# Kernel tuning notes

Hardware: AMD Instinct MI355X
Metric: run time of the kernel (lower is better)

The kernel has to match this reference:

```python
import jax, jax.numpy as jnp
import numpy as np

D_MODEL = 1024
N_HEADS = 16
HEAD_DIM = D_MODEL // N_HEADS


def setup_inputs() -> dict:
    key = jax.random.key(0)
    k0, k1, k2, k3, k4, k5 = jax.random.split(key, 6)
    s = 1.0 / np.sqrt(D_MODEL)
    return {
        "q": jax.random.normal(k0, (2, 2048, D_MODEL), dtype=jnp.float32),
        "Wq": jax.random.normal(k1, (D_MODEL, D_MODEL), dtype=jnp.float32) * s,
        "Wk": jax.random.normal(k2, (D_MODEL, D_MODEL), dtype=jnp.float32) * s,
        "Wv": jax.random.normal(k3, (D_MODEL, D_MODEL), dtype=jnp.float32) * s,
        "Wo": jax.random.normal(k4, (D_MODEL, D_MODEL), dtype=jnp.float32) * s,
        "bo": jax.random.normal(k5, (D_MODEL,), dtype=jnp.float32) * 0.01,
    }


def _split_heads(x):
    b, s, _ = x.shape
    return x.reshape(b, s, N_HEADS, HEAD_DIM).transpose(0, 2, 1, 3)  # [b,h,s,d]


def reference(q, Wq, Wk, Wv, Wo, bo):
    # self-attention: k = v = q
    qh = _split_heads(q @ Wq)  # [b,h,s,d]
    kh = _split_heads(q @ Wk)
    vh = _split_heads(q @ Wv)
    scale = 1.0 / np.sqrt(HEAD_DIM).astype(np.float32)
    scores = jnp.einsum("bhqd,bhkd->bhqk", qh, kh) * scale
    attn = jax.nn.softmax(scores, axis=-1)
    ctx = jnp.einsum("bhqk,bhkd->bhqd", attn, vh)
    b, h, s, d = ctx.shape
    ctx = ctx.transpose(0, 2, 1, 3).reshape(b, s, h * d)
    return ctx @ Wo + bo
```

## Files before the change

### kernel.cpp

```cpp
#include <hip/hip_runtime.h>
#include <cstdint>

typedef unsigned short u16;
typedef __bf16 bf16x8 __attribute__((ext_vector_type(8)));
typedef __bf16 bf16x2 __attribute__((ext_vector_type(2)));
typedef float floatx4 __attribute__((ext_vector_type(4)));
typedef unsigned short u16x4 __attribute__((ext_vector_type(4)));
typedef unsigned short u16x8 __attribute__((ext_vector_type(8)));

#define MFMA16(a, b, c) __builtin_amdgcn_mfma_f32_16x16x32_bf16((a), (b), (c), 0, 0, 0)
#define QSCALE_LOG2E 0.18033688011112042f


typedef __attribute__((address_space(3))) void as3_void;
typedef __attribute__((address_space(1))) void as1_void;

static __device__ __forceinline__ void async_load16(const void* g, void* l) {
  __builtin_amdgcn_global_load_lds((as1_void*)(uintptr_t)g, (as3_void*)(uintptr_t)l,
                                   16, 0, 0);
}

static __device__ __forceinline__ u16 f2bf(float f) {
  union { float f; unsigned int u; } v; v.f = f;
  unsigned int u = v.u;
  u += 0x7fffu + ((u >> 16) & 1u);
  return (u16)(u >> 16);
}

static __device__ __forceinline__ u16x4 pack_bf4(float a, float b, float c, float d) {
#if __has_builtin(__builtin_amdgcn_cvt_pk_bf16_f32)
  union { u16x4 v4; bf16x2 v2[2]; } u;
  u.v2[0] = __builtin_amdgcn_cvt_pk_bf16_f32(a, b);
  u.v2[1] = __builtin_amdgcn_cvt_pk_bf16_f32(c, d);
  return u.v4;
#else
  u16x4 r; r[0] = f2bf(a); r[1] = f2bf(b); r[2] = f2bf(c); r[3] = f2bf(d);
  return r;
#endif
}

static __device__ __forceinline__ float fast_exp2(float x) {
#if __has_builtin(__builtin_amdgcn_exp2f)
  return __builtin_amdgcn_exp2f(x);
#else
  return exp2f(x);
#endif
}


__global__ __launch_bounds__(256) void prep_kernel(
    const float* __restrict__ w0, const float* __restrict__ w1,
    const float* __restrict__ w2, const float* __restrict__ w3,
    u16* __restrict__ wout,
    const float* __restrict__ xin, u16* __restrict__ xout) {
  if (blockIdx.z == 4) {
    int blk = blockIdx.y * 16 + blockIdx.x;
    size_t base = (size_t)blk * 16384 + (size_t)threadIdx.x * 8;
#pragma unroll
    for (int r = 0; r < 8; r++) {
      size_t i = base + (size_t)r * 2048;
      float4 a = *(const float4*)(xin + i);
      float4 b = *(const float4*)(xin + i + 4);
      u16x8 o;
      o[0] = f2bf(a.x); o[1] = f2bf(a.y); o[2] = f2bf(a.z); o[3] = f2bf(a.w);
      o[4] = f2bf(b.x); o[5] = f2bf(b.y); o[6] = f2bf(b.z); o[7] = f2bf(b.w);
      *(u16x8*)(xout + i) = o;
    }
    return;
  }
  __shared__ u16 t[64][65];
  const float* in = (blockIdx.z == 0) ? w0 : (blockIdx.z == 1) ? w1
                    : (blockIdx.z == 2) ? w2 : w3;
  u16* oz = wout + (size_t)blockIdx.z * (1024 * 1024);
  const int tid = threadIdx.x;
  const int x = tid & 63, y0 = tid >> 6;
  const int bx = blockIdx.x * 64, by = blockIdx.y * 64;
#pragma unroll
  for (int p = 0; p < 16; p++) {
    int y = y0 + p * 4;
    t[y][x] = f2bf(in[(size_t)(by + y) * 1024 + bx + x]);
  }
  __syncthreads();
#pragma unroll
  for (int p = 0; p < 16; p++) {
    int r = y0 + p * 4;
    oz[(size_t)(bx + r) * 1024 + by + x] = t[x][r];
  }
}


__global__ __launch_bounds__(256, 3) void gemm_qkv_kernel(
    const u16* __restrict__ A, const u16* __restrict__ BT,
    u16* __restrict__ out, u16* __restrict__ outVT) {
  __shared__ u16 As[128 * 32];
  __shared__ u16 Bs[128 * 32];
  __shared__ u16 tb[64 * 136];
  const int tid = threadIdx.x;
  const int w = tid >> 6, lane = tid & 63;
  const int bm = blockIdx.y * 128, bn = blockIdx.x * 128;
  const int z = blockIdx.z;
  const int K = 1024, N = 1024;
  const u16* Bz = BT + (size_t)z * N * K;

  const int c0 = w * 2, c1 = c0 + 1;
  const int mA0 = c0 * 16 + (lane >> 2), mA1 = c1 * 16 + (lane >> 2);
  const int kg0 = (lane & 3) ^ ((mA0 >> 1) & 3);
  const int kg1 = (lane & 3) ^ ((mA1 >> 1) & 3);
  const u16* agp0 = A + (size_t)(bm + mA0) * K + kg0 * 8;
  const u16* agp1 = A + (size_t)(bm + mA1) * K + kg1 * 8;
  const u16* bgp0 = Bz + (size_t)(bn + mA0) * K + kg0 * 8;
  const u16* bgp1 = Bz + (size_t)(bn + mA1) * K + kg1 * 8;
  u16* ald0 = As + c0 * 512; u16* ald1 = As + c1 * 512;
  u16* bld0 = Bs + c0 * 512; u16* bld1 = Bs + c1 * 512;

  const int wm = (w >> 1) * 64, wn = (w & 1) * 64;
  floatx4 acc[4][4] = {};

  int a_off[4], b_off[4];
#pragma unroll
  for (int i = 0; i < 4; i++) {
    int m = wm + i * 16 + (lane & 15);
    a_off[i] = m * 32 + (((lane >> 4) ^ ((m >> 1) & 3)) * 8);
    int n = wn + i * 16 + (lane & 15);
    b_off[i] = n * 32 + (((lane >> 4) ^ ((n >> 1) & 3)) * 8);
  }

  for (int k0 = 0; k0 < K; k0 += 32) {
    __syncthreads();
    async_load16(agp0 + k0, ald0);
    async_load16(agp1 + k0, ald1);
    async_load16(bgp0 + k0, bld0);
    async_load16(bgp1 + k0, bld1);
    __syncthreads();
    bf16x8 af[4], bf[4];
#pragma unroll
    for (int i = 0; i < 4; i++) af[i] = *(const bf16x8*)(As + a_off[i]);
#pragma unroll
    for (int j = 0; j < 4; j++) bf[j] = *(const bf16x8*)(Bs + b_off[j]);
#pragma unroll
    for (int i = 0; i < 4; i++)
#pragma unroll
      for (int j = 0; j < 4; j++)
        acc[i][j] = MFMA16(af[i], bf[j], acc[i][j]);
  }

  const int roff = (lane >> 4) * 4;
  const int coff = lane & 15;
  if (z == 2) {
    const int b = bm >> 11, s0 = bm & 2047;
#pragma unroll
    for (int half = 0; half < 2; half++) {
      __syncthreads();
      if ((w & 1) == half) {
#pragma unroll
        for (int i = 0; i < 4; i++) {
          int s_local = wm + i * 16 + roff;
#pragma unroll
          for (int j = 0; j < 4; j++) {
            int c_local = j * 16 + coff;
            u16x4 pk = pack_bf4(acc[i][j][0], acc[i][j][1],
                                acc[i][j][2], acc[i][j][3]);
            *(u16x4*)(tb + c_local * 136 + s_local) = pk;
          }
        }
      }
      __syncthreads();
#pragma unroll
      for (int p = 0; p < 4; p++) {
        int c_local = (tid >> 4) & 15;
        int row = p * 16 + c_local;
        int so = tid & 15;
        int cg = bn + half * 64 + row;
        int h = cg >> 6, d = cg & 63;
        u16x8 vv = *(const u16x8*)(tb + row * 136 + so * 8);
        *(u16x8*)(outVT + ((size_t)(b * 16 + h) * 64 + d) * 2048 + s0 + so * 8) = vv;
      }
    }
  } else {
    const float sc = (z == 0) ? QSCALE_LOG2E : 1.0f;
    u16* outz = out + (size_t)z * 4096 * 1024;
#pragma unroll
    for (int i = 0; i < 4; i++) {
      int r0 = bm + wm + i * 16 + roff;
#pragma unroll
      for (int j = 0; j < 4; j++) {
        int c = bn + wn + j * 16 + coff;
#pragma unroll
        for (int r = 0; r < 4; r++)
          outz[(size_t)(r0 + r) * N + c] = f2bf(acc[i][j][r] * sc);
      }
    }
  }
}


__global__ __launch_bounds__(256, 2) void gemm_o_kernel(
    const u16* __restrict__ A, const u16* __restrict__ BT,
    const float* __restrict__ bias, float* __restrict__ out) {
  __shared__ u16 As[128 * 32];
  __shared__ u16 Bs[64 * 32];
  const int tid = threadIdx.x;
  const int w = tid >> 6, lane = tid & 63;
  const int bm = blockIdx.y * 128, bn = blockIdx.x * 64;
  const int K = 1024, N = 1024;

  const u16* gp[3]; u16* ld[3];
#pragma unroll
  for (int i = 0; i < 3; i++) {
    int c = w * 3 + i;
    if (c < 8) {
      int m = c * 16 + (lane >> 2);
      int kg = (lane & 3) ^ ((m >> 1) & 3);
      gp[i] = A + (size_t)(bm + m) * K + kg * 8;
      ld[i] = As + c * 512;
    } else {
      int cb = c - 8;
      int n = cb * 16 + (lane >> 2);
      int kg = (lane & 3) ^ ((n >> 1) & 3);
      gp[i] = BT + (size_t)(bn + n) * K + kg * 8;
      ld[i] = Bs + cb * 512;
    }
  }

  const int wm = (w >> 1) * 64, wn = (w & 1) * 32;
  floatx4 acc[4][2] = {};

  int a_off[4], b_off[2];
#pragma unroll
  for (int i = 0; i < 4; i++) {
    int m = wm + i * 16 + (lane & 15);
    a_off[i] = m * 32 + (((lane >> 4) ^ ((m >> 1) & 3)) * 8);
  }
#pragma unroll
  for (int j = 0; j < 2; j++) {
    int n = wn + j * 16 + (lane & 15);
    b_off[j] = n * 32 + (((lane >> 4) ^ ((n >> 1) & 3)) * 8);
  }

  for (int k0 = 0; k0 < K; k0 += 32) {
    __syncthreads();
    async_load16(gp[0] + k0, ld[0]);
    async_load16(gp[1] + k0, ld[1]);
    async_load16(gp[2] + k0, ld[2]);
    __syncthreads();
    bf16x8 af[4], bf[2];
#pragma unroll
    for (int i = 0; i < 4; i++) af[i] = *(const bf16x8*)(As + a_off[i]);
#pragma unroll
    for (int j = 0; j < 2; j++) bf[j] = *(const bf16x8*)(Bs + b_off[j]);
#pragma unroll
    for (int i = 0; i < 4; i++)
#pragma unroll
      for (int j = 0; j < 2; j++)
        acc[i][j] = MFMA16(af[i], bf[j], acc[i][j]);
  }

  const int roff = (lane >> 4) * 4;
  const int coff = lane & 15;
#pragma unroll
  for (int i = 0; i < 4; i++) {
    int r0 = bm + wm + i * 16 + roff;
#pragma unroll
    for (int j = 0; j < 2; j++) {
      int c = bn + wn + j * 16 + coff;
      float bv = bias[c];
#pragma unroll
      for (int r = 0; r < 4; r++)
        out[(size_t)(r0 + r) * N + c] = acc[i][j][r] + bv;
    }
  }
}


__global__ __launch_bounds__(256, 3) void attn_kernel(
    const u16* __restrict__ Q, const u16* __restrict__ Kx,
    const u16* __restrict__ VT, u16* __restrict__ ctx) {
  __shared__ u16 Ks[128 * 64];
  __shared__ u16 Vs[64 * 128];
  __shared__ u16 Ps[4][32 * 72];
  const int tid = threadIdx.x;
  const int w = tid >> 6, lane = tid & 63;
  const int bid = blockIdx.x;
  const int bh = (bid >> 7) * 8 + (bid & 7);
  const int q0 = ((bid >> 3) & 15) * 128;
  const int b = bh >> 4, h = bh & 15;
  const u16* Qh = Q + (size_t)b * 2048 * 1024 + h * 64;
  const u16* Kh = Kx + (size_t)b * 2048 * 1024 + h * 64;
  const u16* Vh = VT + (size_t)bh * 64 * 2048;

  const int qbase = q0 + w * 32;
  bf16x8 qf[2][2];
#pragma unroll
  for (int qt = 0; qt < 2; qt++)
#pragma unroll
    for (int ks = 0; ks < 2; ks++)
      qf[qt][ks] = *(const bf16x8*)(Qh + (size_t)(qbase + qt * 16 + (lane & 15)) * 1024 +
                                    ks * 32 + (lane >> 4) * 8);

  bf16x8 onesf;
#pragma unroll
  for (int i = 0; i < 8; i++) onesf[i] = (__bf16)1.0f;
  const floatx4 zero4 = {};

  const u16* kgp[4]; const u16* vgp[4];
  u16* kld[4]; u16* vld[4];
#pragma unroll
  for (int i = 0; i < 4; i++) {
    int c = w * 4 + i;
    int sl = c * 8 + (lane >> 3);
    int dg = (lane & 7) ^ (lane >> 3);
    kgp[i] = Kh + (size_t)sl * 1024 + dg * 8;
    kld[i] = Ks + c * 512;
    int dl = c * 4 + (lane >> 4);
    int sg = (lane & 15) ^ (dl & 15);
    vgp[i] = Vh + (size_t)dl * 2048 + sg * 8;
    vld[i] = Vs + c * 512;
  }

  const int slot_k0 = (lane >> 4) ^ (lane & 7);
  const int slot_k1 = (4 + (lane >> 4)) ^ (lane & 7);
  const u16* kf0_base = Ks + (lane & 15) * 64 + slot_k0 * 8;
  const u16* kf1_base = Ks + (lane & 15) * 64 + slot_k1 * 8;

  floatx4 o[2][4] = {};
  floatx4 lacc[2] = {};
  u16* Pw = Ps[w];
  const int qrow0 = (lane & 15) * 72;
  const int qrow1 = (16 + (lane & 15)) * 72;
  const int quad = lane >> 4;

  for (int t = 0; t < 16; t++) {
    const int k0 = t * 128;
    __syncthreads();
#pragma unroll
    for (int i = 0; i < 4; i++) {
      async_load16(kgp[i] + (size_t)k0 * 1024, kld[i]);
      async_load16(vgp[i] + k0, vld[i]);
    }
    __syncthreads();

#pragma unroll
    for (int hh = 0; hh < 2; hh++) {
      floatx4 st0[4], st1[4];
#pragma unroll
      for (int si4 = 0; si4 < 4; si4++) {
        int si = hh * 4 + si4;
        bf16x8 kf0 = *(const bf16x8*)(kf0_base + si * 1024);
        bf16x8 kf1 = *(const bf16x8*)(kf1_base + si * 1024);
        st0[si4] = MFMA16(kf1, qf[0][1], MFMA16(kf0, qf[0][0], zero4));
        st1[si4] = MFMA16(kf1, qf[1][1], MFMA16(kf0, qf[1][0], zero4));
      }
#pragma unroll
      for (int si4 = 0; si4 < 4; si4++) {
        u16x4 pk0 = pack_bf4(fast_exp2(st0[si4][0]), fast_exp2(st0[si4][1]),
                             fast_exp2(st0[si4][2]), fast_exp2(st0[si4][3]));
        u16x4 pk1 = pack_bf4(fast_exp2(st1[si4][0]), fast_exp2(st1[si4][1]),
                             fast_exp2(st1[si4][2]), fast_exp2(st1[si4][3]));
        *(u16x4*)(Pw + qrow0 + si4 * 16 + quad * 4) = pk0;
        *(u16x4*)(Pw + qrow1 + si4 * 16 + quad * 4) = pk1;
      }
#pragma unroll
      for (int ksl = 0; ksl < 2; ksl++) {
        int kb = hh * 2 + ksl;
        bf16x8 vf[4];
#pragma unroll
        for (int jt = 0; jt < 4; jt++) {
          int d = jt * 16 + (lane & 15);
          int slot = (kb * 4 + quad) ^ (d & 15);
          vf[jt] = *(const bf16x8*)(Vs + d * 128 + slot * 8);
        }
#pragma unroll
        for (int qt = 0; qt < 2; qt++) {
          bf16x8 pf = *(const bf16x8*)(Pw + (qt * 16 + (lane & 15)) * 72 +
                                       ksl * 32 + quad * 8);
#pragma unroll
          for (int jt = 0; jt < 4; jt++)
            o[qt][jt] = MFMA16(pf, vf[jt], o[qt][jt]);
          lacc[qt] = MFMA16(pf, onesf, lacc[qt]);
        }
      }
    }
  }

#pragma unroll
  for (int qt = 0; qt < 2; qt++)
#pragma unroll
    for (int r = 0; r < 4; r++) {
      float inv = 1.0f / lacc[qt][r];
      int s = qbase + qt * 16 + quad * 4 + r;
#pragma unroll
      for (int j = 0; j < 4; j++) {
        int c = h * 64 + j * 16 + (lane & 15);
        ctx[(size_t)(b * 2048 + s) * 1024 + c] = f2bf(o[qt][j][r] * inv);
      }
    }
}


extern "C" void kernel_launch(void* const* d_in, const int* in_sizes, int n_in,
                              void* d_out, int out_size, void* d_ws, size_t ws_size,
                              hipStream_t stream) {
  (void)in_sizes; (void)n_in; (void)out_size; (void)ws_size;
  const float* x  = (const float*)d_in[0];
  const float* Wq = (const float*)d_in[1];
  const float* Wk = (const float*)d_in[2];
  const float* Wv = (const float*)d_in[3];
  const float* Wo = (const float*)d_in[4];
  const float* bo = (const float*)d_in[5];
  u16* ws = (u16*)d_ws;
  const size_t MM = 1024 * 1024;
  u16* WT  = ws;
  u16* WoT = ws + 3 * MM;
  u16* Xb  = ws + 4 * MM;
  u16* QKV = ws + 8 * MM;
  u16* VTp = ws + 20 * MM;
  u16* CTX = ws + 24 * MM;

  dim3 blk(256);
  prep_kernel<<<dim3(16, 16, 5), blk, 0, stream>>>(Wq, Wk, Wv, Wo, WT, x, Xb);
  gemm_qkv_kernel<<<dim3(8, 32, 3), blk, 0, stream>>>(Xb, WT, QKV, VTp);
  attn_kernel<<<dim3(512, 1, 1), blk, 0, stream>>>(QKV, QKV + 4 * MM, VTp, CTX);
  gemm_o_kernel<<<dim3(16, 32, 1), blk, 0, stream>>>(CTX, WoT, bo, (float*)d_out);
}
```

Measured before the change: 186.4 us.

## Prefetch next K/V tile into registers while computing current tile

Replaces the synchronous global-to-LDS async loads at the top of each iteration with register prefetching. The next tile's K and V are loaded into registers before compute and written to LDS after it, so global memory latency can overlap with the MFMA work. The extra live registers lead to lowering the launch bounds occupancy hint from 3 to 2 blocks per CU. Fewer resident waves reduces latency hiding from other blocks.

```diff
diff --git a/kernel.cpp b/kernel.cpp
--- a/kernel.cpp
+++ b/kernel.cpp
@@ -272,7 +272,7 @@
 }
 
 
-__global__ __launch_bounds__(256, 3) void attn_kernel(
+__global__ __launch_bounds__(256, 2) void attn_kernel(
     const u16* __restrict__ Q, const u16* __restrict__ Kx,
     const u16* __restrict__ VT, u16* __restrict__ ctx) {
   __shared__ u16 Ks[128 * 64];
@@ -310,11 +310,11 @@
     int sl = c * 8 + (lane >> 3);
     int dg = (lane & 7) ^ (lane >> 3);
     kgp[i] = Kh + (size_t)sl * 1024 + dg * 8;
-    kld[i] = Ks + c * 512;
+    kld[i] = Ks + c * 512 + lane * 8;
     int dl = c * 4 + (lane >> 4);
     int sg = (lane & 15) ^ (dl & 15);
     vgp[i] = Vh + (size_t)dl * 2048 + sg * 8;
-    vld[i] = Vs + c * 512;
+    vld[i] = Vs + c * 512 + lane * 8;
   }
 
   const int slot_k0 = (lane >> 4) ^ (lane & 7);
@@ -329,15 +329,28 @@
   const int qrow1 = (16 + (lane & 15)) * 72;
   const int quad = lane >> 4;
 
+  u16x8 kreg[4], vreg[4];
+#pragma unroll
+  for (int i = 0; i < 4; i++) {
+    kreg[i] = *(const u16x8*)(kgp[i]);
+    vreg[i] = *(const u16x8*)(vgp[i]);
+  }
+#pragma unroll
+  for (int i = 0; i < 4; i++) {
+    *(u16x8*)(kld[i]) = kreg[i];
+    *(u16x8*)(vld[i]) = vreg[i];
+  }
+  __syncthreads();
+
   for (int t = 0; t < 16; t++) {
-    const int k0 = t * 128;
-    __syncthreads();
-#pragma unroll
-    for (int i = 0; i < 4; i++) {
-      async_load16(kgp[i] + (size_t)k0 * 1024, kld[i]);
-      async_load16(vgp[i] + k0, vld[i]);
-    }
-    __syncthreads();
+    if (t < 15) {
+      const size_t k1 = (size_t)(t + 1) * 128;
+#pragma unroll
+      for (int i = 0; i < 4; i++) {
+        kreg[i] = *(const u16x8*)(kgp[i] + k1 * 1024);
+        vreg[i] = *(const u16x8*)(vgp[i] + k1);
+      }
+    }
 
 #pragma unroll
     for (int hh = 0; hh < 2; hh++) {
@@ -379,6 +392,16 @@
           lacc[qt] = MFMA16(pf, onesf, lacc[qt]);
         }
       }
+    }
+
+    if (t < 15) {
+      __syncthreads();
+#pragma unroll
+      for (int i = 0; i < 4; i++) {
+        *(u16x8*)(kld[i]) = kreg[i];
+        *(u16x8*)(vld[i]) = vreg[i];
+      }
+      __syncthreads();
     }
   }
 
```

Result: no change. 187.2 us (+0.4%).

## Split attention work across warps by query and key halves with LDS reduction

Applied to the files above, without the earlier changes.

Each warp now handles 64 query rows against half of the 128-key tile, instead of 32 query rows against the full tile. Partial O and row-sum accumulators from the two key-half warps are combined through LDS at the end. The point is to raise reuse of each K/V fragment read from LDS across more query tiles, cutting LDS reads per MFMA. In exchange register pressure roughly doubles (occupancy hint drops from 3 to 2 blocks), and the epilogue gains an extra LDS reduction and barrier.

```diff
diff --git a/kernel.cpp b/kernel.cpp
--- a/kernel.cpp
+++ b/kernel.cpp
@@ -272,14 +272,16 @@
 }
 
 
-__global__ __launch_bounds__(256, 3) void attn_kernel(
+__global__ __launch_bounds__(256, 2) void attn_kernel(
     const u16* __restrict__ Q, const u16* __restrict__ Kx,
     const u16* __restrict__ VT, u16* __restrict__ ctx) {
-  __shared__ u16 Ks[128 * 64];
-  __shared__ u16 Vs[64 * 128];
-  __shared__ u16 Ps[4][32 * 72];
+  __shared__ __align__(16) u16 lds[8192 + 8192 + 4 * 64 * 68];
+  u16* Ks = lds;
+  u16* Vs = lds + 8192;
+  u16* Ps = lds + 16384;
   const int tid = threadIdx.x;
   const int w = tid >> 6, lane = tid & 63;
+  const int qh = w >> 1, sh = w & 1;
   const int bid = blockIdx.x;
   const int bh = (bid >> 7) * 8 + (bid & 7);
   const int q0 = ((bid >> 3) & 15) * 128;
@@ -287,15 +289,16 @@
   const u16* Qh = Q + (size_t)b * 2048 * 1024 + h * 64;
   const u16* Kh = Kx + (size_t)b * 2048 * 1024 + h * 64;
   const u16* Vh = VT + (size_t)bh * 64 * 2048;
-
-  const int qbase = q0 + w * 32;
-  bf16x8 qf[2][2];
-#pragma unroll
-  for (int qt = 0; qt < 2; qt++)
+  const int quad = lane >> 4;
+
+  const int qbase = q0 + qh * 64;
+  bf16x8 qf[4][2];
+#pragma unroll
+  for (int qt = 0; qt < 4; qt++)
 #pragma unroll
     for (int ks = 0; ks < 2; ks++)
       qf[qt][ks] = *(const bf16x8*)(Qh + (size_t)(qbase + qt * 16 + (lane & 15)) * 1024 +
-                                    ks * 32 + (lane >> 4) * 8);
+                                    ks * 32 + quad * 8);
 
   bf16x8 onesf;
 #pragma unroll
@@ -311,89 +314,111 @@
     int dg = (lane & 7) ^ (lane >> 3);
     kgp[i] = Kh + (size_t)sl * 1024 + dg * 8;
     kld[i] = Ks + c * 512;
-    int dl = c * 4 + (lane >> 4);
+    int dl = c * 4 + quad;
     int sg = (lane & 15) ^ (dl & 15);
     vgp[i] = Vh + (size_t)dl * 2048 + sg * 8;
     vld[i] = Vs + c * 512;
   }
 
-  const int slot_k0 = (lane >> 4) ^ (lane & 7);
-  const int slot_k1 = (4 + (lane >> 4)) ^ (lane & 7);
-  const u16* kf0_base = Ks + (lane & 15) * 64 + slot_k0 * 8;
-  const u16* kf1_base = Ks + (lane & 15) * 64 + slot_k1 * 8;
-
-  floatx4 o[2][4] = {};
-  floatx4 lacc[2] = {};
-  u16* Pw = Ps[w];
-  const int qrow0 = (lane & 15) * 72;
-  const int qrow1 = (16 + (lane & 15)) * 72;
-  const int quad = lane >> 4;
+  const int slot_k0 = quad ^ (lane & 7);
+  const int slot_k1 = (4 + quad) ^ (lane & 7);
+  const u16* kf0_base = Ks + sh * 4096 + (lane & 15) * 64 + slot_k0 * 8;
+  const u16* kf1_base = Ks + sh * 4096 + (lane & 15) * 64 + slot_k1 * 8;
+
+  floatx4 o[4][4] = {};
+  floatx4 lacc[4] = {};
+  u16* Pw = Ps + w * (64 * 68);
+  int qrow[4];
+#pragma unroll
+  for (int qt = 0; qt < 4; qt++) qrow[qt] = (qt * 16 + (lane & 15)) * 68;
 
   for (int t = 0; t < 16; t++) {
-    const int k0 = t * 128;
+    const size_t k0 = (size_t)t * 128;
     __syncthreads();
 #pragma unroll
     for (int i = 0; i < 4; i++) {
-      async_load16(kgp[i] + (size_t)k0 * 1024, kld[i]);
+      async_load16(kgp[i] + k0 * 1024, kld[i]);
       async_load16(vgp[i] + k0, vld[i]);
     }
     __syncthreads();
 
-#pragma unroll
-    for (int hh = 0; hh < 2; hh++) {
-      floatx4 st0[4], st1[4];
-#pragma unroll
-      for (int si4 = 0; si4 < 4; si4++) {
-        int si = hh * 4 + si4;
-        bf16x8 kf0 = *(const bf16x8*)(kf0_base + si * 1024);
-        bf16x8 kf1 = *(const bf16x8*)(kf1_base + si * 1024);
-        st0[si4] = MFMA16(kf1, qf[0][1], MFMA16(kf0, qf[0][0], zero4));
-        st1[si4] = MFMA16(kf1, qf[1][1], MFMA16(kf0, qf[1][0], zero4));
-      }
-#pragma unroll
-      for (int si4 = 0; si4 < 4; si4++) {
-        u16x4 pk0 = pack_bf4(fast_exp2(st0[si4][0]), fast_exp2(st0[si4][1]),
-                             fast_exp2(st0[si4][2]), fast_exp2(st0[si4][3]));
-        u16x4 pk1 = pack_bf4(fast_exp2(st1[si4][0]), fast_exp2(st1[si4][1]),
-                             fast_exp2(st1[si4][2]), fast_exp2(st1[si4][3]));
-        *(u16x4*)(Pw + qrow0 + si4 * 16 + quad * 4) = pk0;
-        *(u16x4*)(Pw + qrow1 + si4 * 16 + quad * 4) = pk1;
-      }
-#pragma unroll
-      for (int ksl = 0; ksl < 2; ksl++) {
-        int kb = hh * 2 + ksl;
-        bf16x8 vf[4];
-#pragma unroll
-        for (int jt = 0; jt < 4; jt++) {
-          int d = jt * 16 + (lane & 15);
-          int slot = (kb * 4 + quad) ^ (d & 15);
-          vf[jt] = *(const bf16x8*)(Vs + d * 128 + slot * 8);
+    floatx4 st[4][4];
+#pragma unroll
+    for (int si = 0; si < 4; si++) {
+      bf16x8 kf0 = *(const bf16x8*)(kf0_base + si * 1024);
+      bf16x8 kf1 = *(const bf16x8*)(kf1_base + si * 1024);
+#pragma unroll
+      for (int qt = 0; qt < 4; qt++)
+        st[si][qt] = MFMA16(kf1, qf[qt][1], MFMA16(kf0, qf[qt][0], zero4));
+    }
+#pragma unroll
+    for (int si = 0; si < 4; si++)
+#pragma unroll
+      for (int qt = 0; qt < 4; qt++) {
+        u16x4 pk = pack_bf4(fast_exp2(st[si][qt][0]), fast_exp2(st[si][qt][1]),
+                            fast_exp2(st[si][qt][2]), fast_exp2(st[si][qt][3]));
+        *(u16x4*)(Pw + qrow[qt] + si * 16 + quad * 4) = pk;
+      }
+
+#pragma unroll
+    for (int ksl = 0; ksl < 2; ksl++) {
+      int kb = sh * 2 + ksl;
+      bf16x8 vf[4];
+#pragma unroll
+      for (int jt = 0; jt < 4; jt++) {
+        int d = jt * 16 + (lane & 15);
+        int slot = (kb * 4 + quad) ^ (d & 15);
+        vf[jt] = *(const bf16x8*)(Vs + d * 128 + slot * 8);
+      }
+#pragma unroll
+      for (int qt = 0; qt < 4; qt++) {
+        bf16x8 pf = *(const bf16x8*)(Pw + qrow[qt] + ksl * 32 + quad * 8);
+#pragma unroll
+        for (int jt = 0; jt < 4; jt++)
+          o[qt][jt] = MFMA16(pf, vf[jt], o[qt][jt]);
+        lacc[qt] = MFMA16(pf, onesf, lacc[qt]);
+      }
+    }
+  }
+
+  __syncthreads();
+  floatx4* dump  = (floatx4*)lds;
+  floatx4* ldump = (floatx4*)(lds + 16384);
+  if (sh == 1) {
+    int base = qh * 1024;
+#pragma unroll
+    for (int qt = 0; qt < 4; qt++)
+#pragma unroll
+      for (int jt = 0; jt < 4; jt++)
+        dump[base + (qt * 4 + jt) * 64 + lane] = o[qt][jt];
+#pragma unroll
+    for (int i = 0; i < 4; i++)
+      ldump[qh * 256 + i * 64 + lane] = lacc[i];
+  }
+  __syncthreads();
+  if (sh == 0) {
+    int base = qh * 1024;
+#pragma unroll
+    for (int qt = 0; qt < 4; qt++)
+#pragma unroll
+      for (int jt = 0; jt < 4; jt++)
+        o[qt][jt] += dump[base + (qt * 4 + jt) * 64 + lane];
+#pragma unroll
+    for (int i = 0; i < 4; i++)
+      lacc[i] += ldump[qh * 256 + i * 64 + lane];
+#pragma unroll
+    for (int qt = 0; qt < 4; qt++)
+#pragma unroll
+      for (int r = 0; r < 4; r++) {
+        float inv = 1.0f / lacc[qt][r];
+        int s = qbase + qt * 16 + quad * 4 + r;
+#pragma unroll
+        for (int j = 0; j < 4; j++) {
+          int c = h * 64 + j * 16 + (lane & 15);
+          ctx[(size_t)(b * 2048 + s) * 1024 + c] = f2bf(o[qt][j][r] * inv);
         }
-#pragma unroll
-        for (int qt = 0; qt < 2; qt++) {
-          bf16x8 pf = *(const bf16x8*)(Pw + (qt * 16 + (lane & 15)) * 72 +
-                                       ksl * 32 + quad * 8);
-#pragma unroll
-          for (int jt = 0; jt < 4; jt++)
-            o[qt][jt] = MFMA16(pf, vf[jt], o[qt][jt]);
-          lacc[qt] = MFMA16(pf, onesf, lacc[qt]);
-        }
-      }
-    }
-  }
-
-#pragma unroll
-  for (int qt = 0; qt < 2; qt++)
-#pragma unroll
-    for (int r = 0; r < 4; r++) {
-      float inv = 1.0f / lacc[qt][r];
-      int s = qbase + qt * 16 + quad * 4 + r;
-#pragma unroll
-      for (int j = 0; j < 4; j++) {
-        int c = h * 64 + j * 16 + (lane & 15);
-        ctx[(size_t)(b * 2048 + s) * 1024 + c] = f2bf(o[qt][j][r] * inv);
-      }
-    }
+      }
+  }
 }
 
 
```

Measured after the change: 196.2 us. 5.3% more time.
